# Kernel tuning notes

Measured on AMD Instinct MI355X. Metric: run time of the kernel, lower is better.

## Reference

```python
import jax, jax.numpy as jnp
import numpy as np
from jax import lax

NPOINT = 1024
NSAMPLE = 32
RADIUS = 0.2
EPS = 1e-5  # BatchNorm eps (torch default)


def farthest_point_sample(xyz, npoint):
    # xyz: [B, N, 3] -> [B, npoint] int32 indices. Deterministic start at index 0
    # (torch version uses a random start; math is otherwise identical).
    B, N, _ = xyz.shape

    def step(carry, _):
        distance, farthest = carry
        centroid = jnp.take_along_axis(xyz, farthest[:, None, None], axis=1)  # [B,1,3]
        d = jnp.sum((xyz - centroid) ** 2, axis=-1)                            # [B,N]
        distance = jnp.minimum(distance, d)
        return (distance, jnp.argmax(distance, axis=-1).astype(jnp.int32)), farthest

    init = (jnp.full((B, N), 1e10, xyz.dtype), jnp.zeros((B,), jnp.int32))
    _, cents = lax.scan(step, init, None, length=npoint)  # [npoint, B]
    return cents.T


def query_ball_point(radius, nsample, xyz, new_xyz):
    # xyz: [B,N,3], new_xyz: [B,S,3] -> [B,S,nsample] int32 indices
    B, N, _ = xyz.shape
    S = new_xyz.shape[1]
    sqr = jnp.sum((new_xyz[:, :, None, :] - xyz[:, None, :, :]) ** 2, axis=-1)  # [B,S,N]
    base = jnp.broadcast_to(jnp.arange(N, dtype=jnp.int32), (B, S, N))
    idx = jnp.where(sqr > radius * radius, N, base)
    idx = jnp.sort(idx, axis=-1)[:, :, :nsample]
    first = idx[:, :, :1]
    return jnp.where(idx == N, first, idx)


def index_points(points, idx):
    # points: [B,N,C], idx: [B,...] -> [B,...,C]
    return jax.vmap(lambda p, i: p[i])(points, idx)


def conv_bn_relu(x, w, b, g, beta):
    # 1x1 Conv2d == per-point linear; BatchNorm2d in training mode (batch stats,
    # biased variance) over all dims except channel.
    y = jnp.einsum('bskc,oc->bsko', x, w) + b          # [B,S,K,O]
    m = jnp.mean(y, axis=(0, 1, 2), keepdims=True)
    v = jnp.var(y, axis=(0, 1, 2), keepdims=True)
    return jax.nn.relu((y - m) / jnp.sqrt(v + EPS) * g + beta)


def setup_inputs() -> dict:
    key = jax.random.key(0)
    ks = jax.random.split(key, 8)
    B, N, D = 16, 4096, 64
    xyz = jax.random.uniform(ks[0], (B, N, 3), dtype=jnp.float32)
    points = jax.random.normal(ks[1], (B, N, D), dtype=jnp.float32)
    chans = [D + 3, 64, 64, 128]
    inp = {'xyz': xyz, 'points': points}
    for i in range(3):
        cin, cout = chans[i], chans[i + 1]
        inp[f'w{i}'] = jax.random.normal(ks[2 + i], (cout, cin), dtype=jnp.float32) * (1.0 / np.sqrt(cin))
        inp[f'b{i}'] = jnp.zeros((cout,), jnp.float32)
        inp[f'g{i}'] = jnp.ones((cout,), jnp.float32)
        inp[f'be{i}'] = jnp.zeros((cout,), jnp.float32)
    return inp


def reference(xyz, points, w0, b0, g0, be0, w1, b1, g1, be1, w2, b2, g2, be2):
    fps_idx = farthest_point_sample(xyz, NPOINT)            # [B,S]
    new_xyz = index_points(xyz, fps_idx)                    # [B,S,3]
    group_idx = query_ball_point(RADIUS, NSAMPLE, xyz, new_xyz)  # [B,S,K]
    grouped_xyz = index_points(xyz, group_idx) - new_xyz[:, :, None, :]  # [B,S,K,3]
    feats = jnp.concatenate([grouped_xyz, index_points(points, group_idx)], axis=-1)
    for (w, b, g, be) in ((w0, b0, g0, be0), (w1, b1, g1, be1), (w2, b2, g2, be2)):
        feats = conv_bn_relu(feats, w, b, g, be)
    new_points = jnp.max(feats, axis=2)                     # max over nsample -> [B,S,C_out]
    return new_xyz, new_points
```

## Files before the change

### kernel.cpp

```cpp
#include <hip/hip_runtime.h>
#include <hip/hip_bf16.h>
#include <cstdint>
#include <cstddef>

#define NPTS   4096
#define NPT    1024
#define NSAMP  32
#define NBATCH 16
#define MROWS  (NBATCH*NPT*NSAMP)
#define EPSV   1e-5f

typedef __attribute__((ext_vector_type(8))) short bfrag;
typedef __attribute__((ext_vector_type(4))) float f32x4;

static __device__ __forceinline__ unsigned short f2bf(float f) {
  union { float f; unsigned u; } x; x.f = f;
  unsigned u = x.u;
  u += 0x7FFFu + ((u >> 16) & 1u);
  return (unsigned short)(u >> 16);
}
static __device__ __forceinline__ float bf2f(unsigned short h) {
  union { unsigned u; float f; } x; x.u = ((unsigned)h) << 16;
  return x.f;
}
static __device__ __forceinline__ unsigned cvt_pk_bf16(float lo, float hi) {
  unsigned r;
  asm("v_cvt_pk_bf16_f32 %0, %1, %2" : "=v"(r) : "v"(lo), "v"(hi));
  return r;
}

__global__ __launch_bounds__(256) void prep_kernel(
    const float* __restrict__ w0, const float* __restrict__ w1,
    const float* __restrict__ w2, unsigned short* __restrict__ wb0,
    unsigned short* __restrict__ wb1, unsigned short* __restrict__ wb2) {
  const int tid = threadIdx.x;
  for (int i = tid; i < 64 * 96; i += 256) {
    const int o = i / 96, c = i % 96;
    wb0[i] = (c < 67) ? f2bf(w0[o * 67 + c]) : (unsigned short)0;
  }
  for (int i = tid; i < 64 * 64; i += 256) wb1[i] = f2bf(w1[i]);
  for (int i = tid; i < 128 * 64; i += 256) wb2[i] = f2bf(w2[i]);
}

#define FPS_T 256
#define PPT   (NPTS / FPS_T)

template <int CTRL>
static __device__ __forceinline__ float dpp_max_step(float v) {
  int t = __builtin_amdgcn_update_dpp(0, __float_as_int(v), CTRL, 0xF, 0xF, true);
  return fmaxf(v, __int_as_float(t));
}

__global__ __launch_bounds__(FPS_T) void fps_kernel(
    const float* __restrict__ xyz, float* __restrict__ out_newxyz) {
  __shared__ __align__(16) float xs[NPTS];
  __shared__ __align__(16) float ys[NPTS];
  __shared__ __align__(16) float zs[NPTS];
  __shared__ __align__(16) float olds[NPT * 3];
  __shared__ __align__(16) uint2 sl[2][4];

  const int b = blockIdx.x;
  const int tid = threadIdx.x;
  const int wave = tid >> 6;
  const float* base = xyz + (size_t)b * NPTS * 3;
  for (int i = tid; i < NPTS; i += FPS_T) {
    xs[i] = base[3 * i + 0];
    ys[i] = base[3 * i + 1];
    zs[i] = base[3 * i + 2];
  }
  __syncthreads();

  const int p0 = tid * PPT;
  float px[PPT], py[PPT], pz[PPT], dist[PPT];
  #pragma unroll
  for (int i = 0; i < PPT; i += 4) {
    *(float4*)&px[i] = *(const float4*)&xs[p0 + i];
    *(float4*)&py[i] = *(const float4*)&ys[p0 + i];
    *(float4*)&pz[i] = *(const float4*)&zs[p0 + i];
  }
  #pragma unroll
  for (int i = 0; i < PPT; ++i) dist[i] = 1e10f;

  int cur = 0;
  for (int it = 0; it < NPT; ++it) {
    const float cx = xs[cur], cy = ys[cur], cz = zs[cur];
    if (tid == 0) {
      olds[3 * it + 0] = cx;
      olds[3 * it + 1] = cy;
      olds[3 * it + 2] = cz;
    }
    if (it == NPT - 1) break;

    float bestv = -1.f; int besti = p0;
    #pragma unroll
    for (int i = 0; i < PPT; ++i) {
      const float dx = __fsub_rn(px[i], cx);
      const float dy = __fsub_rn(py[i], cy);
      const float dz = __fsub_rn(pz[i], cz);
      const float d = __fadd_rn(__fadd_rn(__fmul_rn(dx, dx), __fmul_rn(dy, dy)),
                                __fmul_rn(dz, dz));
      const float nd = fminf(dist[i], d);
      dist[i] = nd;
      const bool g = nd > bestv;
      bestv = g ? nd : bestv;
      besti = g ? (p0 + i) : besti;
    }

    float m = bestv;
    m = dpp_max_step<0x111>(m);
    m = dpp_max_step<0x112>(m);
    m = dpp_max_step<0x114>(m);
    m = dpp_max_step<0x118>(m);
    m = dpp_max_step<0x142>(m);
    m = dpp_max_step<0x143>(m);
    const float wmax =
        __int_as_float(__builtin_amdgcn_readlane(__float_as_int(m), 63));

    const unsigned long long mask = __ballot(bestv == wmax);
    const int wl = __ffsll((long long)mask) - 1;
    const int widx = __builtin_amdgcn_readlane(besti, wl);

    const int buf = it & 1;
    if ((tid & 63) == 0)
      sl[buf][wave] = make_uint2(__float_as_uint(wmax), (unsigned)widx);
    __syncthreads();

    const uint4* p4 = (const uint4*)&sl[buf][0];
    const uint4 q0 = p4[0], q1 = p4[1];
    float bv; int bi;
    {
      bv = __uint_as_float(q0.x); bi = (int)q0.y;
      const float v1 = __uint_as_float(q0.z);
      if (v1 > bv) { bv = v1; bi = (int)q0.w; }
      const float v2 = __uint_as_float(q1.x);
      if (v2 > bv) { bv = v2; bi = (int)q1.y; }
      const float v3 = __uint_as_float(q1.z);
      if (v3 > bv) { bv = v3; bi = (int)q1.w; }
    }
    cur = bi;
  }

  __syncthreads();
  float* outb = out_newxyz + (size_t)b * NPT * 3;
  for (int i = tid; i < NPT * 3 / 4; i += FPS_T)
    *(float4*)&outb[4 * i] = *(const float4*)&olds[4 * i];
}

__global__ __launch_bounds__(256) void ballquery_kernel(
    const float* __restrict__ xyz, const float* __restrict__ newxyz,
    int* __restrict__ gidx) {
  const int gw = (int)((blockIdx.x * 256 + threadIdx.x) >> 6);
  const int lane = threadIdx.x & 63;
  const int b = gw >> 10, s = gw & 1023;
  const float* base = xyz + (size_t)b * NPTS * 3;
  const float* c = newxyz + (size_t)(b * NPT + s) * 3;
  const float cx = c[0], cy = c[1], cz = c[2];
  const float R2 = (float)(0.2 * 0.2);
  int* g = gidx + (size_t)(b * NPT + s) * NSAMP;

  int count = 0;
  int first = -1;
  for (int ch = 0; ch < NPTS / 64; ++ch) {
    const int i = ch * 64 + lane;
    const float dx = __fsub_rn(base[3 * i + 0], cx);
    const float dy = __fsub_rn(base[3 * i + 1], cy);
    const float dz = __fsub_rn(base[3 * i + 2], cz);
    const float d = __fadd_rn(__fadd_rn(__fmul_rn(dx, dx), __fmul_rn(dy, dy)),
                              __fmul_rn(dz, dz));
    const bool pred = !(d > R2);
    const unsigned long long mask = __ballot(pred);
    if (mask) {
      if (count == 0) first = ch * 64 + (__ffsll((long long)mask) - 1);
      const int rank = __popcll(mask & ((1ull << lane) - 1ull));
      const int pos = count + rank;
      if (pred && pos < NSAMP) g[pos] = i;
      count += (int)__popcll(mask);
      if (count >= NSAMP) break;
    }
  }
  if (first < 0) first = 0;
  for (int j = count + lane; j < NSAMP; j += 64) g[j] = first;
}

__global__ __launch_bounds__(256) void mm1_mfma_kernel(
    const float* __restrict__ xyz, const float* __restrict__ points,
    const float* __restrict__ newxyz, const int* __restrict__ gidx,
    const unsigned short* __restrict__ Wb, unsigned short* __restrict__ Y,
    float* __restrict__ psum, float* __restrict__ psq) {
  constexpr int KP = 104;
  __shared__ __align__(16) unsigned short As[64 * KP];
  __shared__ __align__(16) unsigned short ly[64 * 64];
  __shared__ float ssum[64], ssq[64];
  const int tid = threadIdx.x, bid = blockIdx.x;
  const size_t r0 = (size_t)bid * 64;

  {
    const int row = tid >> 2, q = tid & 3;
    const int gs = bid * 2 + (row >> 5);
    const int b = gs >> 10;
    const int k = row & 31;
    const int gpt = gidx[(size_t)gs * NSAMP + k];
    const float* px = xyz + ((size_t)b * NPTS + gpt) * 3;
    const float* pc = newxyz + (size_t)gs * 3;
    const float* pf = points + ((size_t)b * NPTS + gpt) * 64;
    float v[24];
    #pragma unroll
    for (int cc = 0; cc < 24; ++cc) {
      const int cch = q * 24 + cc;
      float val;
      if (cch < 3)       val = px[cch] - pc[cch];
      else if (cch < 67) val = pf[cch - 3];
      else               val = 0.f;
      v[cc] = val;
    }
    unsigned* dst = (unsigned*)&As[row * KP + q * 24];
    #pragma unroll
    for (int p = 0; p < 12; ++p) dst[p] = cvt_pk_bf16(v[2 * p], v[2 * p + 1]);
  }
  if (tid < 64) { ssum[tid] = 0.f; ssq[tid] = 0.f; }
  __syncthreads();

  const int wave = tid >> 6, lane = tid & 63;
  const int l15 = lane & 15, kq = lane >> 4;
  const unsigned short* abase = &As[(wave * 16 + l15) * KP + kq * 8];
  const bfrag a0 = *(const bfrag*)abase;
  const bfrag a1 = *(const bfrag*)(abase + 32);
  const bfrag a2 = *(const bfrag*)(abase + 64);

  #pragma unroll
  for (int nt = 0; nt < 4; ++nt) {
    const unsigned short* wsrc = Wb + (size_t)(nt * 16 + l15) * 96 + kq * 8;
    const bfrag b0 = *(const bfrag*)wsrc;
    const bfrag b1 = *(const bfrag*)(wsrc + 32);
    const bfrag b2 = *(const bfrag*)(wsrc + 64);
    f32x4 acc = {0.f, 0.f, 0.f, 0.f};
    acc = __builtin_amdgcn_mfma_f32_16x16x32_bf16(a0, b0, acc, 0, 0, 0);
    acc = __builtin_amdgcn_mfma_f32_16x16x32_bf16(a1, b1, acc, 0, 0, 0);
    acc = __builtin_amdgcn_mfma_f32_16x16x32_bf16(a2, b2, acc, 0, 0, 0);

    float s = acc[0] + acc[1] + acc[2] + acc[3];
    float q = acc[0]*acc[0] + acc[1]*acc[1] + acc[2]*acc[2] + acc[3]*acc[3];
    s += __shfl_xor(s, 16); q += __shfl_xor(q, 16);
    s += __shfl_xor(s, 32); q += __shfl_xor(q, 32);
    if (kq == 0) {
      atomicAdd(&ssum[nt * 16 + l15], s);
      atomicAdd(&ssq [nt * 16 + l15], q);
    }
    const unsigned p01 = cvt_pk_bf16(acc[0], acc[1]);
    const unsigned p23 = cvt_pk_bf16(acc[2], acc[3]);
    const int colo = nt * 16 + l15;
    const int rbase = wave * 16 + kq * 4;
    ly[(rbase + 0) * 64 + colo] = (unsigned short)(p01 & 0xffffu);
    ly[(rbase + 1) * 64 + colo] = (unsigned short)(p01 >> 16);
    ly[(rbase + 2) * 64 + colo] = (unsigned short)(p23 & 0xffffu);
    ly[(rbase + 3) * 64 + colo] = (unsigned short)(p23 >> 16);
  }
  __syncthreads();
  {
    const uint4* lsrc = (const uint4*)ly;
    uint4* gdst = (uint4*)(Y + r0 * 64);
    #pragma unroll
    for (int i = tid; i < 64 * 64 * 2 / 16; i += 256) gdst[i] = lsrc[i];
  }
  if (tid < 64) {
    psum[(size_t)bid * 64 + tid] = ssum[tid];
    psq [(size_t)bid * 64 + tid] = ssq [tid];
  }
}

static __device__ __forceinline__ bfrag affine_relu_frag(
    const unsigned short* __restrict__ src, const float* __restrict__ st,
    int c0) {
  union { bfrag f; unsigned u[4]; } r;
  const uint4 raw = *(const uint4*)src;
  const unsigned w[4] = {raw.x, raw.y, raw.z, raw.w};
  #pragma unroll
  for (int p = 0; p < 4; ++p) {
    const int c = c0 + 2 * p;
    float lo = bf2f((unsigned short)(w[p] & 0xffffu));
    float hi = bf2f((unsigned short)(w[p] >> 16));
    lo = fmaxf(fmaf(lo, st[2 * c + 0], st[2 * c + 1]), 0.f);
    hi = fmaxf(fmaf(hi, st[2 * c + 2], st[2 * c + 3]), 0.f);
    r.u[p] = cvt_pk_bf16(lo, hi);
  }
  return r.f;
}

template <int COUT, int WAVES>
__global__ __launch_bounds__(WAVES * 64) void mm_mfma_kernel(
    const unsigned short* __restrict__ Xin, const unsigned short* __restrict__ Wb,
    const float* __restrict__ stin, unsigned short* __restrict__ Y,
    float* __restrict__ psum, float* __restrict__ psq) {
  constexpr int NT = COUT / 16;
  constexpr int ROWS = WAVES * 16;
  __shared__ float ssum[COUT], ssq[COUT];
  __shared__ __align__(16) unsigned short ly[ROWS * COUT];
  const int tid = threadIdx.x, bid = blockIdx.x;
  const int wave = tid >> 6, lane = tid & 63;
  const int l15 = lane & 15, kq = lane >> 4;
  const size_t r0 = (size_t)bid * ROWS;
  if (tid < COUT) { ssum[tid] = 0.f; ssq[tid] = 0.f; }

  const int arow = wave * 16 + l15;
  const unsigned short* asrc = Xin + (r0 + arow) * 64 + kq * 8;
  const bfrag a0 = affine_relu_frag(asrc, stin, kq * 8);
  const bfrag a1 = affine_relu_frag(asrc + 32, stin, 32 + kq * 8);
  __syncthreads();

  #pragma unroll
  for (int nt = 0; nt < NT; ++nt) {
    const unsigned short* wsrc = Wb + (size_t)(nt * 16 + l15) * 64 + kq * 8;
    const bfrag b0 = *(const bfrag*)wsrc;
    const bfrag b1 = *(const bfrag*)(wsrc + 32);
    f32x4 acc = {0.f, 0.f, 0.f, 0.f};
    acc = __builtin_amdgcn_mfma_f32_16x16x32_bf16(a0, b0, acc, 0, 0, 0);
    acc = __builtin_amdgcn_mfma_f32_16x16x32_bf16(a1, b1, acc, 0, 0, 0);

    float s = acc[0] + acc[1] + acc[2] + acc[3];
    float q = acc[0]*acc[0] + acc[1]*acc[1] + acc[2]*acc[2] + acc[3]*acc[3];
    s += __shfl_xor(s, 16); q += __shfl_xor(q, 16);
    s += __shfl_xor(s, 32); q += __shfl_xor(q, 32);
    if (kq == 0) {
      atomicAdd(&ssum[nt * 16 + l15], s);
      atomicAdd(&ssq [nt * 16 + l15], q);
    }
    const unsigned p01 = cvt_pk_bf16(acc[0], acc[1]);
    const unsigned p23 = cvt_pk_bf16(acc[2], acc[3]);
    const int colo = nt * 16 + l15;
    const int rbase = wave * 16 + kq * 4;
    ly[(rbase + 0) * COUT + colo] = (unsigned short)(p01 & 0xffffu);
    ly[(rbase + 1) * COUT + colo] = (unsigned short)(p01 >> 16);
    ly[(rbase + 2) * COUT + colo] = (unsigned short)(p23 & 0xffffu);
    ly[(rbase + 3) * COUT + colo] = (unsigned short)(p23 >> 16);
  }
  __syncthreads();
  {
    const uint4* lsrc = (const uint4*)ly;
    uint4* gdst = (uint4*)(Y + r0 * COUT);
    #pragma unroll
    for (int i = tid; i < ROWS * COUT * 2 / 16; i += WAVES * 64) gdst[i] = lsrc[i];
  }
  if (tid < COUT) {
    psum[(size_t)bid * COUT + tid] = ssum[tid];
    psq [(size_t)bid * COUT + tid] = ssq [tid];
  }
}

__global__ __launch_bounds__(512) void mm3_pool_kernel(
    const unsigned short* __restrict__ Xin, const unsigned short* __restrict__ Wb,
    const float* __restrict__ stin, float* __restrict__ pooled,
    float* __restrict__ psum, float* __restrict__ psq) {
  constexpr int COUT = 128, NT = 8;
  __shared__ float ssum[COUT], ssq[COUT];
  __shared__ float pm[8][COUT];
  const int tid = threadIdx.x, bid = blockIdx.x;
  const int wave = tid >> 6, lane = tid & 63;
  const int l15 = lane & 15, kq = lane >> 4;
  const size_t r0 = (size_t)bid * 128;
  if (tid < COUT) { ssum[tid] = 0.f; ssq[tid] = 0.f; }

  const int arow = wave * 16 + l15;
  const unsigned short* asrc = Xin + (r0 + arow) * 64 + kq * 8;
  const bfrag a0 = affine_relu_frag(asrc, stin, kq * 8);
  const bfrag a1 = affine_relu_frag(asrc + 32, stin, 32 + kq * 8);
  __syncthreads();

  #pragma unroll
  for (int nt = 0; nt < NT; ++nt) {
    const unsigned short* wsrc = Wb + (size_t)(nt * 16 + l15) * 64 + kq * 8;
    const bfrag b0 = *(const bfrag*)wsrc;
    const bfrag b1 = *(const bfrag*)(wsrc + 32);
    f32x4 acc = {0.f, 0.f, 0.f, 0.f};
    acc = __builtin_amdgcn_mfma_f32_16x16x32_bf16(a0, b0, acc, 0, 0, 0);
    acc = __builtin_amdgcn_mfma_f32_16x16x32_bf16(a1, b1, acc, 0, 0, 0);

    float s = acc[0] + acc[1] + acc[2] + acc[3];
    float q = acc[0]*acc[0] + acc[1]*acc[1] + acc[2]*acc[2] + acc[3]*acc[3];
    s += __shfl_xor(s, 16); q += __shfl_xor(q, 16);
    s += __shfl_xor(s, 32); q += __shfl_xor(q, 32);
    float mx = fmaxf(fmaxf(acc[0], acc[1]), fmaxf(acc[2], acc[3]));
    mx = fmaxf(mx, __shfl_xor(mx, 16));
    mx = fmaxf(mx, __shfl_xor(mx, 32));
    if (kq == 0) {
      atomicAdd(&ssum[nt * 16 + l15], s);
      atomicAdd(&ssq [nt * 16 + l15], q);
      pm[wave][nt * 16 + l15] = mx;
    }
  }
  __syncthreads();
  {
    const int g = tid >> 7, col = tid & 127;
    const float v = fmaxf(pm[2 * g][col], pm[2 * g + 1][col]);
    pooled[(r0 >> 5) * COUT + g * COUT + col] = v;
  }
  if (tid < COUT) {
    psum[(size_t)bid * COUT + tid] = ssum[tid];
    psq [(size_t)bid * COUT + tid] = ssq [tid];
  }
}

__global__ __launch_bounds__(256) void finalize_kernel(
    const float* __restrict__ psum, const float* __restrict__ psq,
    const float* __restrict__ gam, const float* __restrict__ bet,
    float* __restrict__ st, int C, int nb) {
  const int c = blockIdx.x, tid = threadIdx.x;
  float s = 0.f, q = 0.f;
  for (int i = tid; i < nb; i += 256) {
    s += psum[(size_t)i * C + c];
    q += psq [(size_t)i * C + c];
  }
  #pragma unroll
  for (int off = 32; off > 0; off >>= 1) {
    s += __shfl_down(s, off);
    q += __shfl_down(q, off);
  }
  __shared__ float as_[4], aq_[4];
  if ((tid & 63) == 0) { as_[tid >> 6] = s; aq_[tid >> 6] = q; }
  __syncthreads();
  if (tid == 0) {
    s = as_[0] + as_[1] + as_[2] + as_[3];
    q = aq_[0] + aq_[1] + aq_[2] + aq_[3];
    const float invM = 1.f / (float)MROWS;
    const float mean = s * invM;
    const float var = q * invM - mean * mean;
    const float inv = 1.f / sqrtf(var + EPSV);
    const float sc = gam[c] * inv;
    st[2 * c + 0] = sc;
    st[2 * c + 1] = bet[c] - mean * sc;
  }
}

__global__ __launch_bounds__(256) void bn_relu_kernel(
    const float* __restrict__ pooled, const float* __restrict__ st,
    float* __restrict__ out) {
  __shared__ float s_st[256];
  const int tid = threadIdx.x;
  s_st[tid] = st[tid];
  __syncthreads();
  const int n4 = NBATCH * NPT * 128 / 4;
  for (int i = blockIdx.x * 256 + tid; i < n4; i += gridDim.x * 256) {
    float4 v = ((const float4*)pooled)[i];
    const int c0 = (i * 4) & 127;
    v.x = fmaxf(fmaf(v.x, s_st[2 * c0 + 0], s_st[2 * c0 + 1]), 0.f);
    v.y = fmaxf(fmaf(v.y, s_st[2 * c0 + 2], s_st[2 * c0 + 3]), 0.f);
    v.z = fmaxf(fmaf(v.z, s_st[2 * c0 + 4], s_st[2 * c0 + 5]), 0.f);
    v.w = fmaxf(fmaf(v.w, s_st[2 * c0 + 6], s_st[2 * c0 + 7]), 0.f);
    ((float4*)out)[i] = v;
  }
}

extern "C" void kernel_launch(void* const* d_in, const int* in_sizes, int n_in,
                              void* d_out, int out_size, void* d_ws, size_t ws_size,
                              hipStream_t stream) {
  (void)in_sizes; (void)n_in; (void)out_size; (void)ws_size;
  const float* xyz    = (const float*)d_in[0];
  const float* points = (const float*)d_in[1];
  const float* w0 = (const float*)d_in[2];
  const float* g0 = (const float*)d_in[4];
  const float* be0 = (const float*)d_in[5];
  const float* w1 = (const float*)d_in[6];
  const float* g1 = (const float*)d_in[8];
  const float* be1 = (const float*)d_in[9];
  const float* w2 = (const float*)d_in[10];
  const float* g2 = (const float*)d_in[12];
  const float* be2 = (const float*)d_in[13];

  float* out = (float*)d_out;
  float* newxyz = out;
  float* newpts = out + (size_t)NBATCH * NPT * 3;

  char* ws = (char*)d_ws;
  unsigned short* Y1 = (unsigned short*)ws;
  float* P3 = (float*)ws;
  unsigned short* Y2 = (unsigned short*)(ws + 134217728);
  int*   gidx = (int*)  (ws + 201326592);
  float* psum = (float*)(ws + 203423744);
  float* psq  = (float*)(ws + 205520896);
  float* st   = (float*)(ws + 207618048);
  float* st1 = st, *st2 = st + 256, *st3 = st + 512;
  unsigned short* wb0 = (unsigned short*)(ws + 207621120);
  unsigned short* wb1 = (unsigned short*)(ws + 207621120 + 12288);
  unsigned short* wb2 = (unsigned short*)(ws + 207621120 + 12288 + 8192);

  prep_kernel<<<1, 256, 0, stream>>>(w0, w1, w2, wb0, wb1, wb2);
  fps_kernel<<<NBATCH, FPS_T, 0, stream>>>(xyz, newxyz);
  ballquery_kernel<<<(NBATCH * NPT) / 4, 256, 0, stream>>>(xyz, newxyz, gidx);
  mm1_mfma_kernel<<<MROWS / 64, 256, 0, stream>>>(xyz, points, newxyz, gidx, wb0, Y1, psum, psq);
  finalize_kernel<<<64, 256, 0, stream>>>(psum, psq, g0, be0, st1, 64, MROWS / 64);
  mm_mfma_kernel<64, 4><<<MROWS / 64, 256, 0, stream>>>(Y1, wb1, st1, Y2, psum, psq);
  finalize_kernel<<<64, 256, 0, stream>>>(psum, psq, g1, be1, st2, 64, MROWS / 64);
  mm3_pool_kernel<<<MROWS / 128, 512, 0, stream>>>(Y2, wb2, st2, P3, psum, psq);
  finalize_kernel<<<128, 256, 0, stream>>>(psum, psq, g2, be2, st3, 128, MROWS / 128);
  bn_relu_kernel<<<2048, 256, 0, stream>>>(P3, st3, newpts);
}
```

Before: 904.4 us.

## Reorder conv0 channels for vector gathers and pack FPS math into float2

The first-layer weight layout is permuted so the 64 point features occupy columns 0-63 and the 3 relative coordinates sit at 64-66. This lets the gather in mm1 use aligned float4 loads and 16-byte LDS stores instead of per-element branchy loads. The FPS inner loop is rewritten on float2 vectors so the compiler can emit packed FP32 ops, with FP contraction disabled to keep rounding unchanged. The risk is that argmax tie-breaking within a pair could differ slightly, and the extra code in the q==0 lane adds divergence.

```diff
diff --git a/kernel.cpp b/kernel.cpp
--- a/kernel.cpp
+++ b/kernel.cpp
@@ -12,6 +12,7 @@
 
 typedef __attribute__((ext_vector_type(8))) short bfrag;
 typedef __attribute__((ext_vector_type(4))) float f32x4;
+typedef __attribute__((ext_vector_type(2))) float f32x2;
 
 static __device__ __forceinline__ unsigned short f2bf(float f) {
   union { float f; unsigned u; } x; x.f = f;
@@ -36,7 +37,11 @@
   const int tid = threadIdx.x;
   for (int i = tid; i < 64 * 96; i += 256) {
     const int o = i / 96, c = i % 96;
-    wb0[i] = (c < 67) ? f2bf(w0[o * 67 + c]) : (unsigned short)0;
+    float v;
+    if (c < 64)      v = w0[o * 67 + 3 + c];
+    else if (c < 67) v = w0[o * 67 + (c - 64)];
+    else             v = 0.f;
+    wb0[i] = f2bf(v);
   }
   for (int i = tid; i < 64 * 64; i += 256) wb1[i] = f2bf(w1[i]);
   for (int i = tid; i < 128 * 64; i += 256) wb2[i] = f2bf(w2[i]);
@@ -71,15 +76,14 @@
   __syncthreads();
 
   const int p0 = tid * PPT;
-  float px[PPT], py[PPT], pz[PPT], dist[PPT];
+  f32x2 px2[8], py2[8], pz2[8], d2[8];
   #pragma unroll
-  for (int i = 0; i < PPT; i += 4) {
-    *(float4*)&px[i] = *(const float4*)&xs[p0 + i];
-    *(float4*)&py[i] = *(const float4*)&ys[p0 + i];
-    *(float4*)&pz[i] = *(const float4*)&zs[p0 + i];
-  }
-  #pragma unroll
-  for (int i = 0; i < PPT; ++i) dist[i] = 1e10f;
+  for (int p = 0; p < 8; ++p) {
+    px2[p] = f32x2{xs[p0 + 2 * p], xs[p0 + 2 * p + 1]};
+    py2[p] = f32x2{ys[p0 + 2 * p], ys[p0 + 2 * p + 1]};
+    pz2[p] = f32x2{zs[p0 + 2 * p], zs[p0 + 2 * p + 1]};
+    d2[p] = f32x2{1e10f, 1e10f};
+  }
 
   int cur = 0;
   for (int it = 0; it < NPT; ++it) {
@@ -92,18 +96,26 @@
     if (it == NPT - 1) break;
 
     float bestv = -1.f; int besti = p0;
-    #pragma unroll
-    for (int i = 0; i < PPT; ++i) {
-      const float dx = __fsub_rn(px[i], cx);
-      const float dy = __fsub_rn(py[i], cy);
-      const float dz = __fsub_rn(pz[i], cz);
-      const float d = __fadd_rn(__fadd_rn(__fmul_rn(dx, dx), __fmul_rn(dy, dy)),
-                                __fmul_rn(dz, dz));
-      const float nd = fminf(dist[i], d);
-      dist[i] = nd;
-      const bool g = nd > bestv;
-      bestv = g ? nd : bestv;
-      besti = g ? (p0 + i) : besti;
+    {
+      #pragma clang fp contract(off)
+      const f32x2 c2x = {cx, cx}, c2y = {cy, cy}, c2z = {cz, cz};
+      #pragma unroll
+      for (int p = 0; p < 8; ++p) {
+        const f32x2 dx = px2[p] - c2x;
+        const f32x2 dy = py2[p] - c2y;
+        const f32x2 dz = pz2[p] - c2z;
+        const f32x2 s = (dx * dx + dy * dy) + dz * dz;
+        f32x2 nd = d2[p];
+        nd.x = fminf(nd.x, s.x);
+        nd.y = fminf(nd.y, s.y);
+        d2[p] = nd;
+        const float pmax = fmaxf(nd.x, nd.y);
+        const bool yg = nd.y > nd.x;
+        const int pidx = p0 + 2 * p + (yg ? 1 : 0);
+        const bool g = pmax > bestv;
+        bestv = g ? pmax : bestv;
+        besti = g ? pidx : besti;
+      }
     }
 
     float m = bestv;
@@ -200,22 +212,30 @@
     const int b = gs >> 10;
     const int k = row & 31;
     const int gpt = gidx[(size_t)gs * NSAMP + k];
-    const float* px = xyz + ((size_t)b * NPTS + gpt) * 3;
-    const float* pc = newxyz + (size_t)gs * 3;
-    const float* pf = points + ((size_t)b * NPTS + gpt) * 64;
-    float v[24];
+    const float* pf = points + ((size_t)b * NPTS + gpt) * 64 + 16 * q;
+    float f[16];
     #pragma unroll
-    for (int cc = 0; cc < 24; ++cc) {
-      const int cch = q * 24 + cc;
-      float val;
-      if (cch < 3)       val = px[cch] - pc[cch];
-      else if (cch < 67) val = pf[cch - 3];
-      else               val = 0.f;
-      v[cc] = val;
-    }
-    unsigned* dst = (unsigned*)&As[row * KP + q * 24];
-    #pragma unroll
-    for (int p = 0; p < 12; ++p) dst[p] = cvt_pk_bf16(v[2 * p], v[2 * p + 1]);
+    for (int i = 0; i < 4; ++i)
+      *(float4*)&f[4 * i] = *(const float4*)&pf[4 * i];
+    uint4 u0, u1;
+    u0.x = cvt_pk_bf16(f[0], f[1]);   u0.y = cvt_pk_bf16(f[2], f[3]);
+    u0.z = cvt_pk_bf16(f[4], f[5]);   u0.w = cvt_pk_bf16(f[6], f[7]);
+    u1.x = cvt_pk_bf16(f[8], f[9]);   u1.y = cvt_pk_bf16(f[10], f[11]);
+    u1.z = cvt_pk_bf16(f[12], f[13]); u1.w = cvt_pk_bf16(f[14], f[15]);
+    uint4* dst = (uint4*)&As[row * KP + 16 * q];
+    dst[0] = u0; dst[1] = u1;
+    if (q == 0) {
+      const float* px = xyz + ((size_t)b * NPTS + gpt) * 3;
+      const float* pc = newxyz + (size_t)gs * 3;
+      const float rx = px[0] - pc[0];
+      const float ry = px[1] - pc[1];
+      const float rz = px[2] - pc[2];
+      uint4* d2 = (uint4*)&As[row * KP + 64];
+      d2[0] = uint4{cvt_pk_bf16(rx, ry), cvt_pk_bf16(rz, 0.f), 0u, 0u};
+      d2[1] = uint4{0u, 0u, 0u, 0u};
+      d2[2] = uint4{0u, 0u, 0u, 0u};
+      d2[3] = uint4{0u, 0u, 0u, 0u};
+    }
   }
   if (tid < 64) { ssum[tid] = 0.f; ssq[tid] = 0.f; }
   __syncthreads();
```

Result: faster. 863.4 us (-4.5%).

## Fuse ball query into first MFMA layer and pre-convert points to bf16

Applied to the files above, without the earlier changes.

Removes the separate ball-query kernel. Its group indices are now computed inside mm1 by two waves per block and held in LDS, so the global gidx round trip and one launch disappear. Points are converted to bf16 once by a new prep kernel, and the weight columns are reordered so the 64 feature channels come first. This lets the gather copy aligned 16-byte bf16 chunks instead of scalar fp32 loads followed by conversion. The cost is that the other two waves sit idle during the ball query, which runs serially inside each mm1 block, and the extra conversion pass reads the full points array.

```diff
diff --git a/kernel.cpp b/kernel.cpp
--- a/kernel.cpp
+++ b/kernel.cpp
@@ -36,10 +36,23 @@
   const int tid = threadIdx.x;
   for (int i = tid; i < 64 * 96; i += 256) {
     const int o = i / 96, c = i % 96;
-    wb0[i] = (c < 67) ? f2bf(w0[o * 67 + c]) : (unsigned short)0;
+    float v;
+    if (c < 64)      v = w0[o * 67 + 3 + c];
+    else if (c < 67) v = w0[o * 67 + (c - 64)];
+    else             v = 0.f;
+    wb0[i] = f2bf(v);
   }
   for (int i = tid; i < 64 * 64; i += 256) wb1[i] = f2bf(w1[i]);
   for (int i = tid; i < 128 * 64; i += 256) wb2[i] = f2bf(w2[i]);
+}
+
+__global__ __launch_bounds__(256) void prep_points_kernel(
+    const float* __restrict__ points, unsigned short* __restrict__ pointsb) {
+  const int n2 = NBATCH * NPTS * 64 / 2;
+  for (int i = blockIdx.x * 256 + threadIdx.x; i < n2; i += gridDim.x * 256) {
+    const float2 v = ((const float2*)points)[i];
+    ((unsigned*)pointsb)[i] = cvt_pk_bf16(v.x, v.y);
+  }
 }
 
 #define FPS_T 256
@@ -146,81 +159,83 @@
     *(float4*)&outb[4 * i] = *(const float4*)&olds[4 * i];
 }
 
-__global__ __launch_bounds__(256) void ballquery_kernel(
-    const float* __restrict__ xyz, const float* __restrict__ newxyz,
-    int* __restrict__ gidx) {
-  const int gw = (int)((blockIdx.x * 256 + threadIdx.x) >> 6);
-  const int lane = threadIdx.x & 63;
-  const int b = gw >> 10, s = gw & 1023;
-  const float* base = xyz + (size_t)b * NPTS * 3;
-  const float* c = newxyz + (size_t)(b * NPT + s) * 3;
-  const float cx = c[0], cy = c[1], cz = c[2];
-  const float R2 = (float)(0.2 * 0.2);
-  int* g = gidx + (size_t)(b * NPT + s) * NSAMP;
-
-  int count = 0;
-  int first = -1;
-  for (int ch = 0; ch < NPTS / 64; ++ch) {
-    const int i = ch * 64 + lane;
-    const float dx = __fsub_rn(base[3 * i + 0], cx);
-    const float dy = __fsub_rn(base[3 * i + 1], cy);
-    const float dz = __fsub_rn(base[3 * i + 2], cz);
-    const float d = __fadd_rn(__fadd_rn(__fmul_rn(dx, dx), __fmul_rn(dy, dy)),
-                              __fmul_rn(dz, dz));
-    const bool pred = !(d > R2);
-    const unsigned long long mask = __ballot(pred);
-    if (mask) {
-      if (count == 0) first = ch * 64 + (__ffsll((long long)mask) - 1);
-      const int rank = __popcll(mask & ((1ull << lane) - 1ull));
-      const int pos = count + rank;
-      if (pred && pos < NSAMP) g[pos] = i;
-      count += (int)__popcll(mask);
-      if (count >= NSAMP) break;
-    }
-  }
-  if (first < 0) first = 0;
-  for (int j = count + lane; j < NSAMP; j += 64) g[j] = first;
-}
-
 __global__ __launch_bounds__(256) void mm1_mfma_kernel(
-    const float* __restrict__ xyz, const float* __restrict__ points,
-    const float* __restrict__ newxyz, const int* __restrict__ gidx,
-    const unsigned short* __restrict__ Wb, unsigned short* __restrict__ Y,
-    float* __restrict__ psum, float* __restrict__ psq) {
+    const float* __restrict__ xyz, const unsigned short* __restrict__ pointsb,
+    const float* __restrict__ newxyz, const unsigned short* __restrict__ Wb,
+    unsigned short* __restrict__ Y, float* __restrict__ psum,
+    float* __restrict__ psq) {
   constexpr int KP = 104;
   __shared__ __align__(16) unsigned short As[64 * KP];
   __shared__ __align__(16) unsigned short ly[64 * 64];
   __shared__ float ssum[64], ssq[64];
+  __shared__ int   gidxL[64];
+  __shared__ float cents[8];
   const int tid = threadIdx.x, bid = blockIdx.x;
+  const int wave = tid >> 6, lane = tid & 63;
   const size_t r0 = (size_t)bid * 64;
+  const int b = (bid * 2) >> 10;
+
+  if (wave < 2) {
+    const int gs = bid * 2 + wave;
+    const float* base = xyz + (size_t)b * NPTS * 3;
+    const float* c = newxyz + (size_t)gs * 3;
+    const float cx = c[0], cy = c[1], cz = c[2];
+    if (lane == 0) {
+      cents[wave * 4 + 0] = cx;
+      cents[wave * 4 + 1] = cy;
+      cents[wave * 4 + 2] = cz;
+    }
+    const float R2 = (float)(0.2 * 0.2);
+    int* g = &gidxL[wave * 32];
+    int count = 0;
+    int first = -1;
+    for (int ch = 0; ch < NPTS / 64; ++ch) {
+      const int i = ch * 64 + lane;
+      const float dx = __fsub_rn(base[3 * i + 0], cx);
+      const float dy = __fsub_rn(base[3 * i + 1], cy);
+      const float dz = __fsub_rn(base[3 * i + 2], cz);
+      const float d = __fadd_rn(
+          __fadd_rn(__fmul_rn(dx, dx), __fmul_rn(dy, dy)), __fmul_rn(dz, dz));
+      const bool pred = !(d > R2);
+      const unsigned long long mask = __ballot(pred);
+      if (mask) {
+        if (count == 0) first = ch * 64 + (__ffsll((long long)mask) - 1);
+        const int rank = __popcll(mask & ((1ull << lane) - 1ull));
+        const int pos = count + rank;
+        if (pred && pos < NSAMP) g[pos] = i;
+        count += (int)__popcll(mask);
+        if (count >= NSAMP) break;
+      }
+    }
+    if (first < 0) first = 0;
+    for (int j = count + lane; j < NSAMP; j += 64) g[j] = first;
+  }
+  if (tid < 64) { ssum[tid] = 0.f; ssq[tid] = 0.f; }
+  __syncthreads();
 
   {
     const int row = tid >> 2, q = tid & 3;
-    const int gs = bid * 2 + (row >> 5);
-    const int b = gs >> 10;
-    const int k = row & 31;
-    const int gpt = gidx[(size_t)gs * NSAMP + k];
-    const float* px = xyz + ((size_t)b * NPTS + gpt) * 3;
-    const float* pc = newxyz + (size_t)gs * 3;
-    const float* pf = points + ((size_t)b * NPTS + gpt) * 64;
-    float v[24];
-    #pragma unroll
-    for (int cc = 0; cc < 24; ++cc) {
-      const int cch = q * 24 + cc;
-      float val;
-      if (cch < 3)       val = px[cch] - pc[cch];
-      else if (cch < 67) val = pf[cch - 3];
-      else               val = 0.f;
-      v[cc] = val;
-    }
-    unsigned* dst = (unsigned*)&As[row * KP + q * 24];
-    #pragma unroll
-    for (int p = 0; p < 12; ++p) dst[p] = cvt_pk_bf16(v[2 * p], v[2 * p + 1]);
-  }
-  if (tid < 64) { ssum[tid] = 0.f; ssq[tid] = 0.f; }
-  __syncthreads();
-
-  const int wave = tid >> 6, lane = tid & 63;
+    const int gpt = gidxL[row];
+    const unsigned short* pf = pointsb + ((size_t)b * NPTS + gpt) * 64 + 16 * q;
+    const uint4 u0 = *(const uint4*)pf;
+    const uint4 u1 = *(const uint4*)(pf + 8);
+    uint4* dst = (uint4*)&As[row * KP + 16 * q];
+    dst[0] = u0; dst[1] = u1;
+    if (q == 0) {
+      const float* px = xyz + ((size_t)b * NPTS + gpt) * 3;
+      const float* pc = &cents[(row >> 5) * 4];
+      const float rx = px[0] - pc[0];
+      const float ry = px[1] - pc[1];
+      const float rz = px[2] - pc[2];
+      uint4* d2 = (uint4*)&As[row * KP + 64];
+      d2[0] = uint4{cvt_pk_bf16(rx, ry), cvt_pk_bf16(rz, 0.f), 0u, 0u};
+      d2[1] = uint4{0u, 0u, 0u, 0u};
+      d2[2] = uint4{0u, 0u, 0u, 0u};
+      d2[3] = uint4{0u, 0u, 0u, 0u};
+    }
+  }
+  __syncthreads();
+
   const int l15 = lane & 15, kq = lane >> 4;
   const unsigned short* abase = &As[(wave * 16 + l15) * KP + kq * 8];
   const bfrag a0 = *(const bfrag*)abase;
@@ -472,8 +487,8 @@
   char* ws = (char*)d_ws;
   unsigned short* Y1 = (unsigned short*)ws;
   float* P3 = (float*)ws;
+  unsigned short* pointsb = (unsigned short*)(ws + 67108864);
   unsigned short* Y2 = (unsigned short*)(ws + 134217728);
-  int*   gidx = (int*)  (ws + 201326592);
   float* psum = (float*)(ws + 203423744);
   float* psq  = (float*)(ws + 205520896);
   float* st   = (float*)(ws + 207618048);
@@ -483,9 +498,9 @@
   unsigned short* wb2 = (unsigned short*)(ws + 207621120 + 12288 + 8192);
 
   prep_kernel<<<1, 256, 0, stream>>>(w0, w1, w2, wb0, wb1, wb2);
+  prep_points_kernel<<<512, 256, 0, stream>>>(points, pointsb);
   fps_kernel<<<NBATCH, FPS_T, 0, stream>>>(xyz, newxyz);
-  ballquery_kernel<<<(NBATCH * NPT) / 4, 256, 0, stream>>>(xyz, newxyz, gidx);
-  mm1_mfma_kernel<<<MROWS / 64, 256, 0, stream>>>(xyz, points, newxyz, gidx, wb0, Y1, psum, psq);
+  mm1_mfma_kernel<<<MROWS / 64, 256, 0, stream>>>(xyz, pointsb, newxyz, wb0, Y1, psum, psq);
   finalize_kernel<<<64, 256, 0, stream>>>(psum, psq, g0, be0, st1, 64, MROWS / 64);
   mm_mfma_kernel<64, 4><<<MROWS / 64, 256, 0, stream>>>(Y1, wb1, st1, Y2, psum, psq);
   finalize_kernel<<<64, 256, 0, stream>>>(psum, psq, g1, be1, st2, 64, MROWS / 64);
```

New measurement: 856.5 us. 5.3% less time.
